# Kernel optimization log

Measured on AMD Instinct MI355X. Metric: run time of the kernel, lower is better.

The kernel has to match this reference:

```python
import jax, jax.numpy as jnp
import numpy as np

EPS = 1e-5


def setup_inputs() -> dict:
    key = jax.random.key(0)
    ks = jax.random.split(key, 16)
    N, P, K, D = 16, 1024, 16, 3
    Cf = 64      # out_features (lifted feature dim)
    Fin = 64     # feature_dim
    Cout = 128   # out_channels
    DM = 4       # depth multiplier
    Ccat = Cf + Fin  # 128
    s = 0.1
    return {
        'rep_pt': jax.random.normal(ks[0], (N, P, D), jnp.float32),
        'pts':    jax.random.normal(ks[1], (N, P, K, D), jnp.float32),
        'fts':    jax.random.normal(ks[2], (N, P, K, Fin), jnp.float32),
        'W_fc1':  jax.random.normal(ks[3], (Cf, D), jnp.float32) * s,
        'b_fc1':  jnp.zeros((Cf,), jnp.float32),
        'W_fc2':  jax.random.normal(ks[4], (Cf, Cf), jnp.float32) * s,
        'b_fc2':  jnp.zeros((Cf,), jnp.float32),
        'W_xconv': jax.random.normal(ks[5], (K * K, D, K), jnp.float32) * s,
        'b_xconv': jnp.zeros((K * K,), jnp.float32),
        'W_xfc1': jax.random.normal(ks[6], (K * K, K * K), jnp.float32) * s,
        'b_xfc1': jnp.zeros((K * K,), jnp.float32),
        'W_xfc2': jax.random.normal(ks[7], (K * K, K * K), jnp.float32) * s,
        'b_xfc2': jnp.zeros((K * K,), jnp.float32),
        'W_dw':   jax.random.normal(ks[8], (Ccat, DM, K), jnp.float32) * s,
        'b_dw':   jnp.zeros((Ccat * DM,), jnp.float32),
        'W_pw':   jax.random.normal(ks[9], (Cout, Ccat * DM), jnp.float32) * s,
        'b_pw':   jnp.zeros((Cout,), jnp.float32),
        'gamma':  jnp.ones((Cout,), jnp.float32),
        'beta':   jnp.zeros((Cout,), jnp.float32),
    }


def reference(rep_pt, pts, fts, W_fc1, b_fc1, W_fc2, b_fc2,
              W_xconv, b_xconv, W_xfc1, b_xfc1, W_xfc2, b_xfc2,
              W_dw, b_dw, W_pw, b_pw, gamma, beta):
    relu = jax.nn.relu
    N, P, K, _ = pts.shape

    # local coords around each representative point
    pts_local = pts - rep_pt[:, :, None, :]                       # (N,P,K,3)

    # feature lift: two FCs with relu
    h = relu(jnp.einsum('npkd,fd->npkf', pts_local, W_fc1) + b_fc1)
    fts_lifted = relu(jnp.einsum('npkf,gf->npkg', h, W_fc2) + b_fc2)  # (N,P,K,Cf)
    fts_cat = jnp.concatenate([fts_lifted, fts], axis=-1)         # (N,P,K,Ccat)

    # X-transform: conv2d kernel (1,K) over (N,3,P,K) -> (N,K^2,P,1), then 2 FCs
    X = relu(jnp.einsum('npkd,odk->npo', pts_local, W_xconv) + b_xconv)  # (N,P,K^2)
    X = relu(X @ W_xfc1.T + b_xfc1)
    X = X @ W_xfc2.T + b_xfc2                                     # linear
    X = X.reshape(N, P, K, K)

    # X-transformed features
    fts_X = jnp.einsum('npij,npjc->npic', X, fts_cat)             # (N,P,K,Ccat)

    # depthwise-separable conv with kernel (1,K): reduces K entirely
    x = fts_X.transpose(0, 3, 1, 2)                               # (N,Ccat,P,K)
    dw = jnp.einsum('ncpk,cmk->ncmp', x, W_dw)                    # (N,Ccat,DM,P)
    dw = dw.reshape(N, -1, P) + b_dw[None, :, None]               # (N,Ccat*DM,P)
    y = jnp.einsum('ncp,oc->nop', dw, W_pw) + b_pw[None, :, None] # (N,Cout,P)

    # batchnorm (training stats over N,P per channel), then relu
    mean = y.mean(axis=(0, 2), keepdims=True)
    var = y.var(axis=(0, 2), keepdims=True)
    y = (y - mean) * jax.lax.rsqrt(var + EPS)
    y = relu(gamma[None, :, None] * y + beta[None, :, None])

    return y.transpose(0, 2, 1)                                   # (N,P,Cout)
```

## Files before the change

### kernel.cpp

```cpp
#include <hip/hip_runtime.h>


#define NPTS 16384

typedef short  s16x8 __attribute__((ext_vector_type(8)));
typedef float  f32x4 __attribute__((ext_vector_type(4)));

__device__ inline unsigned short f2b(float f) {
    unsigned u = __builtin_bit_cast(unsigned, f);
    unsigned r = u + 0x7FFF + ((u >> 16) & 1);
    return (unsigned short)(r >> 16);
}
__device__ inline float b2f(unsigned short b) {
    return __builtin_bit_cast(float, (unsigned)b << 16);
}

#define MFMA(a,b,c) __builtin_amdgcn_mfma_f32_16x16x32_bf16((a),(b),(c),0,0,0)

__global__ __launch_bounds__(256) void kW_cvt(
    const float* __restrict__ Wxc, const float* __restrict__ Wx1,
    const float* __restrict__ Wx2, const float* __restrict__ Wf2,
    const float* __restrict__ Wpw, const float* __restrict__ Wf1,
    const float* __restrict__ bf1, const float* __restrict__ Wdw,
    unsigned short* __restrict__ Wpk, float* __restrict__ W1p,
    unsigned short* __restrict__ Wtb, float* __restrict__ acc)
{
    unsigned short* Wxcpk = Wpk;
    unsigned short* Wx1pk = Wpk + 16384;
    unsigned short* Wx2pk = Wpk + 81920;
    unsigned short* Wf2pk = Wpk + 147456;
    unsigned short* Wpwpk = Wpk + 151552;
    int idx = blockIdx.x * 256 + threadIdx.x;
    if (idx < 16384) {
        int e = idx & 7, ln = (idx >> 3) & 63, ks = (idx >> 9) & 1, ot = idx >> 10;
        int row = ot*16 + (ln & 15), k = ks*32 + (ln >> 4)*8 + e;
        Wxcpk[idx] = (k < 48) ? f2b(Wxc[row*48 + k]) : 0; return; }
    idx -= 16384;
    if (idx < 65536) {
        int e = idx & 7, ln = (idx >> 3) & 63, ks = (idx >> 9) & 7, ot = idx >> 12;
        int row = ot*16 + (ln & 15), k = ks*32 + (ln >> 4)*8 + e;
        Wx1pk[idx] = f2b(Wx1[row*256 + k]); return; }
    idx -= 65536;
    if (idx < 65536) {
        int e = idx & 7, ln = (idx >> 3) & 63, ks = (idx >> 9) & 7, ot = idx >> 12;
        int row = ot*16 + (ln & 15), k = ks*32 + (ln >> 4)*8 + e;
        Wx2pk[idx] = f2b(Wx2[row*256 + k]); return; }
    idx -= 65536;
    if (idx < 4096) {
        int e = idx & 7, ln = (idx >> 3) & 63, ks = (idx >> 9) & 1, ot = idx >> 10;
        int row = ot*16 + (ln & 15), k = ks*32 + (ln >> 4)*8 + e;
        Wf2pk[idx] = f2b(Wf2[row*64 + k]); return; }
    idx -= 4096;
    if (idx < 65536) {
        int e = idx & 7, ln = (idx >> 3) & 63, ks = (idx >> 9) & 15, ot = idx >> 13;
        int row = ot*16 + (ln & 15), k = ks*32 + (ln >> 4)*8 + e;
        Wpwpk[idx] = f2b(Wpw[row*512 + k]); return; }
    idx -= 65536;
    if (idx < 256)   { int f = idx >> 2, j = idx & 3;
        W1p[idx] = (j < 3) ? Wf1[f*3 + j] : bf1[f]; return; }
    idx -= 256;
    if (idx < 8192)  { int m = idx >> 11, rem = idx & 2047;
        int c = rem >> 4, k = rem & 15;
        Wtb[idx] = f2b(Wdw[(size_t)(c*4 + m)*16 + k]); return; }
    idx -= 8192;
    if (idx < 256)   { acc[idx] = 0.f; return; }
}

#define SX 264
__global__ __launch_bounds__(512) void kA_mfma(
    const float* __restrict__ rep, const float* __restrict__ pts,
    const unsigned short* __restrict__ Wpk,
    const float* __restrict__ bxc, const float* __restrict__ bx1,
    const float* __restrict__ bx2, unsigned short* __restrict__ X3b)
{
    const unsigned short* Wxcpk = Wpk;
    const unsigned short* Wx1pk = Wpk + 16384;
    const unsigned short* Wx2pk = Wpk + 81920;
    __shared__ __align__(16) unsigned short X1s[32*SX];
    __shared__ __align__(16) unsigned short X2s[32*SX];
    const int tid = threadIdx.x;
    const int w = tid >> 6, lane = tid & 63, cl = lane & 15, lg = lane >> 4;
    const int mw = w & 1, nw = w >> 1;
    const int base = blockIdx.x * 32;
    const int q = base + mw*16 + cl;
    f32x4 z = {0.f,0.f,0.f,0.f};

    float r0 = rep[q*3+0], r1 = rep[q*3+1], r2 = rep[q*3+2];
    s16x8 aa[2];
    #pragma unroll
    for (int ks = 0; ks < 2; ++ks) {
        #pragma unroll
        for (int e = 0; e < 8; ++e) {
            int j = ks*32 + lg*8 + e;
            float v = 0.f;
            if (j < 48) {
                int d = j >> 4, kk = j & 15;
                float rv = (d == 0) ? r0 : ((d == 1) ? r1 : r2);
                v = pts[(size_t)(q*16 + kk)*3 + d] - rv;
            }
            aa[ks][e] = (short)f2b(v);
        }
    }

    {
        f32x4 acc[4] = {z,z,z,z};
        #pragma unroll
        for (int ks = 0; ks < 2; ++ks) {
            #pragma unroll
            for (int ct = 0; ct < 4; ++ct) {
                int ot = nw*4 + ct;
                s16x8 b = *(const s16x8*)&Wxcpk[((ot*2 + ks)*64 + lane)*8];
                acc[ct] = MFMA(aa[ks], b, acc[ct]);
            }
        }
        #pragma unroll
        for (int ct = 0; ct < 4; ++ct) {
            int o = nw*64 + ct*16 + cl;
            float bias = bxc[o];
            #pragma unroll
            for (int r = 0; r < 4; ++r)
                X1s[(mw*16 + lg*4 + r)*SX + o] = f2b(fmaxf(acc[ct][r] + bias, 0.f));
        }
    }
    __syncthreads();

    {
        f32x4 acc[4] = {z,z,z,z};
        #pragma unroll
        for (int ks = 0; ks < 8; ++ks) {
            s16x8 a = *(const s16x8*)&X1s[(mw*16 + cl)*SX + ks*32 + lg*8];
            #pragma unroll
            for (int ct = 0; ct < 4; ++ct) {
                int ot = nw*4 + ct;
                s16x8 b = *(const s16x8*)&Wx1pk[((ot*8 + ks)*64 + lane)*8];
                acc[ct] = MFMA(a, b, acc[ct]);
            }
        }
        #pragma unroll
        for (int ct = 0; ct < 4; ++ct) {
            int o = nw*64 + ct*16 + cl;
            float bias = bx1[o];
            #pragma unroll
            for (int r = 0; r < 4; ++r)
                X2s[(mw*16 + lg*4 + r)*SX + o] = f2b(fmaxf(acc[ct][r] + bias, 0.f));
        }
    }
    __syncthreads();

    {
        f32x4 acc[4] = {z,z,z,z};
        #pragma unroll
        for (int ks = 0; ks < 8; ++ks) {
            s16x8 a = *(const s16x8*)&X2s[(mw*16 + cl)*SX + ks*32 + lg*8];
            #pragma unroll
            for (int ct = 0; ct < 4; ++ct) {
                int ot = nw*4 + ct;
                s16x8 b = *(const s16x8*)&Wx2pk[((ot*8 + ks)*64 + lane)*8];
                acc[ct] = MFMA(a, b, acc[ct]);
            }
        }
        #pragma unroll
        for (int ct = 0; ct < 4; ++ct) {
            int o = nw*64 + ct*16 + cl;
            float bias = bx2[o];
            #pragma unroll
            for (int r = 0; r < 4; ++r)
                X3b[(size_t)(base + mw*16 + lg*4 + r)*256 + o] = f2b(acc[ct][r] + bias);
        }
    }
}

#define SF 72
__global__ __launch_bounds__(256) void kB_mfma(
    const float* __restrict__ rep, const float* __restrict__ pts,
    const float* __restrict__ fts, const float* __restrict__ W1p,
    const unsigned short* __restrict__ Wpk, const float* __restrict__ bf2,
    const unsigned short* __restrict__ Wtb, const float* __restrict__ bdw,
    const unsigned short* __restrict__ X3b, unsigned short* __restrict__ dwb)
{
    const unsigned short* Wf2pk = Wpk + 147456;
    __shared__ __align__(16) unsigned short fcT[128*SF];
    const int tid = threadIdx.x;
    const int w = tid >> 6, lane = tid & 63, cl = lane & 15, lg = lane >> 4;
    const int p = blockIdx.x*4 + w;
    const int rw = w*16;

    const int frow = lane >> 2, fch = lane & 3;
    float4 fv[4];
    #pragma unroll
    for (int it = 0; it < 4; ++it)
        fv[it] = *(const float4*)&fts[((size_t)p*16 + frow)*64 + fch*4 + it*16];

    s16x8 xa = {0,0,0,0,0,0,0,0};
    if (lg < 2) xa = *(const s16x8*)&X3b[(size_t)p*256 + cl*16 + lg*8];

    const int row = p*16 + cl;
    float x0 = pts[(size_t)row*3+0] - rep[p*3+0];
    float x1 = pts[(size_t)row*3+1] - rep[p*3+1];
    float x2 = pts[(size_t)row*3+2] - rep[p*3+2];

    s16x8 hb[2];
    #pragma unroll
    for (int ks = 0; ks < 2; ++ks) {
        #pragma unroll
        for (int e = 0; e < 8; ++e) {
            int f = ks*32 + lg*8 + e;
            float4 wb4 = *(const float4*)&W1p[f*4];
            float h = fmaxf(wb4.w + wb4.x*x0 + wb4.y*x1 + wb4.z*x2, 0.f);
            hb[ks][e] = (short)f2b(h);
        }
    }

    #pragma unroll
    for (int it = 0; it < 4; ++it) {
        float vv[4] = {fv[it].x, fv[it].y, fv[it].z, fv[it].w};
        #pragma unroll
        for (int cc = 0; cc < 4; ++cc) {
            int c = fch*4 + it*16 + cc;
            fcT[(64 + c)*SF + rw + frow] = f2b(vv[cc]);
        }
    }

    f32x4 z = {0.f,0.f,0.f,0.f};
    {
        f32x4 acc2[4] = {z,z,z,z};
        #pragma unroll
        for (int ks = 0; ks < 2; ++ks) {
            #pragma unroll
            for (int gt = 0; gt < 4; ++gt) {
                s16x8 a = *(const s16x8*)&Wf2pk[((gt*2 + ks)*64 + lane)*8];
                acc2[gt] = MFMA(a, hb[ks], acc2[gt]);
            }
        }
        #pragma unroll
        for (int gt = 0; gt < 4; ++gt) {
            #pragma unroll
            for (int r = 0; r < 4; ++r) {
                int g = gt*16 + lg*4 + r;
                fcT[g*SF + rw + cl] = f2b(fmaxf(acc2[gt][r] + bf2[g], 0.f));
            }
        }
    }

    f32x4 fx[8];
    #pragma unroll
    for (int ct = 0; ct < 8; ++ct) {
        int c = ct*16 + cl;
        s16x8 b = *(const s16x8*)&fcT[c*SF + rw + (lg & 1)*8];
        fx[ct] = MFMA(xa, b, z);
    }

    #pragma unroll
    for (int ct = 0; ct < 8; ++ct) {
        int c = ct*16 + cl;
        float4 b4 = *(const float4*)&bdw[c*4];
        float om[4];
        #pragma unroll
        for (int m = 0; m < 4; ++m) {
            ushort4 wu = *(const ushort4*)&Wtb[m*2048 + c*16 + lg*4];
            float s = fx[ct][0]*b2f(wu.x) + fx[ct][1]*b2f(wu.y)
                    + fx[ct][2]*b2f(wu.z) + fx[ct][3]*b2f(wu.w);
            s += __shfl_xor(s, 16);
            s += __shfl_xor(s, 32);
            om[m] = s + ((const float*)&b4)[m];
        }
        if (lg == 0) {
            ushort4 pk; pk.x=f2b(om[0]); pk.y=f2b(om[1]); pk.z=f2b(om[2]); pk.w=f2b(om[3]);
            *(ushort4*)&dwb[(size_t)p*512 + c*4] = pk;
        }
    }
}

__global__ __launch_bounds__(256) void kC_mfma(
    const unsigned short* __restrict__ dwb, const unsigned short* __restrict__ Wpk,
    const float* __restrict__ bpw, float* __restrict__ y,
    float* __restrict__ accS, float* __restrict__ accS2)
{
    const unsigned short* Wpwpk = Wpk + 151552;
    const int tid = threadIdx.x;
    const int w = tid >> 6, lane = tid & 63, cl = lane & 15, lg = lane >> 4;
    const int m0 = blockIdx.x*32 + (w & 1)*16;
    const int nh = w >> 1;
    f32x4 z = {0.f,0.f,0.f,0.f};
    f32x4 acc[4] = {z,z,z,z};
    for (int ks = 0; ks < 16; ++ks) {
        s16x8 a = *(const s16x8*)&dwb[(size_t)(m0 + cl)*512 + ks*32 + lg*8];
        #pragma unroll
        for (int ct = 0; ct < 4; ++ct) {
            int ot = nh*4 + ct;
            s16x8 b = *(const s16x8*)&Wpwpk[((ot*16 + ks)*64 + lane)*8];
            acc[ct] = MFMA(a, b, acc[ct]);
        }
    }
    #pragma unroll
    for (int ct = 0; ct < 4; ++ct) {
        int o = nh*64 + ct*16 + cl;
        float bias = bpw[o];
        float s1 = 0.f, s2 = 0.f;
        #pragma unroll
        for (int r = 0; r < 4; ++r) {
            float v = acc[ct][r] + bias;
            y[(size_t)(m0 + lg*4 + r)*128 + o] = v;
            s1 += v; s2 += v*v;
        }
        s1 += __shfl_xor(s1, 16); s2 += __shfl_xor(s2, 16);
        s1 += __shfl_xor(s1, 32); s2 += __shfl_xor(s2, 32);
        if (lg == 0) {
            atomicAdd(accS + o, s1);
            atomicAdd(accS2 + o, s2);
        }
    }
}

__global__ void kD2_fin(
    const float* __restrict__ accS, const float* __restrict__ accS2,
    const float* __restrict__ gamma, const float* __restrict__ beta,
    float* __restrict__ st)
{
    const int c = threadIdx.x;
    float mean = accS[c] * (1.f/NPTS);
    float var  = accS2[c] * (1.f/NPTS) - mean*mean;
    float rstd = rsqrtf(var + 1e-5f);
    float sc = gamma[c] * rstd;
    st[c] = sc;
    st[128 + c] = beta[c] - mean*sc;
}

__global__ __launch_bounds__(256) void kE_final(
    const float* __restrict__ y, const float* __restrict__ st,
    float* __restrict__ out)
{
    const int idx = blockIdx.x*256 + threadIdx.x;
    float4 v = ((const float4*)y)[idx];
    int o0 = (idx & 31) << 2;
    float4 sc = *(const float4*)(st + o0);
    float4 sh = *(const float4*)(st + 128 + o0);
    float4 r;
    r.x = fmaxf(v.x*sc.x + sh.x, 0.f);
    r.y = fmaxf(v.y*sc.y + sh.y, 0.f);
    r.z = fmaxf(v.z*sc.z + sh.z, 0.f);
    r.w = fmaxf(v.w*sc.w + sh.w, 0.f);
    ((float4*)out)[idx] = r;
}

extern "C" void kernel_launch(void* const* d_in, const int* in_sizes, int n_in,
                              void* d_out, int out_size, void* d_ws, size_t ws_size,
                              hipStream_t stream) {
    const float* rep  = (const float*)d_in[0];
    const float* pts  = (const float*)d_in[1];
    const float* fts  = (const float*)d_in[2];
    const float* Wf1  = (const float*)d_in[3];
    const float* bf1  = (const float*)d_in[4];
    const float* Wf2  = (const float*)d_in[5];
    const float* bf2  = (const float*)d_in[6];
    const float* Wxc  = (const float*)d_in[7];
    const float* bxc  = (const float*)d_in[8];
    const float* Wx1  = (const float*)d_in[9];
    const float* bx1  = (const float*)d_in[10];
    const float* Wx2  = (const float*)d_in[11];
    const float* bx2  = (const float*)d_in[12];
    const float* Wdw  = (const float*)d_in[13];
    const float* bdw  = (const float*)d_in[14];
    const float* Wpw  = (const float*)d_in[15];
    const float* bpw  = (const float*)d_in[16];
    const float* gam  = (const float*)d_in[17];
    const float* bet  = (const float*)d_in[18];

    unsigned short* X3b = (unsigned short*)d_ws;
    unsigned short* dwb = X3b + (size_t)NPTS*256;
    float* y   = (float*)(dwb + (size_t)NPTS*512);
    float* st  = y + (size_t)NPTS*128;
    float* acc = st + 256;
    unsigned short* Wpk = (unsigned short*)(acc + 256);
    float* W1p = (float*)(Wpk + 217088);
    unsigned short* Wtb = (unsigned short*)(W1p + 256);

    kW_cvt<<<882, 256, 0, stream>>>(Wxc, Wx1, Wx2, Wf2, Wpw, Wf1, bf1, Wdw,
                                    Wpk, W1p, Wtb, acc);
    kA_mfma<<<NPTS/32, 512, 0, stream>>>(rep, pts, Wpk, bxc, bx1, bx2, X3b);
    kB_mfma<<<NPTS/4, 256, 0, stream>>>(rep, pts, fts, W1p, Wpk, bf2, Wtb, bdw, X3b, dwb);
    kC_mfma<<<NPTS/32, 256, 0, stream>>>(dwb, Wpk, bpw, y, acc, acc + 128);
    kD2_fin<<<1, 128, 0, stream>>>(acc, acc + 128, gam, bet, st);
    kE_final<<<(NPTS*128/4)/256, 256, 0, stream>>>(y, st, (float*)d_out);
}
```

Before: 120.7 us.

## Use packed bf16 conversion, fuse BN finalize into apply kernel, interleave kB MFMA

Replaces the software float-to-bf16 rounding with the hardware v_cvt_pk_bf16_f32 instruction, which converts two values at once, in kA and kB. It folds the single-block batchnorm-stats kernel into the final apply kernel so every block recomputes scale and shift into shared memory, removing one launch. In kB it also interleaves the per-channel-tile MFMA with its depthwise reduction so the eight MFMA results are no longer all held in registers together. The aim is to cut conversion ALU work, one launch and register pressure, at the cost of redundant per-block stats math.

```diff
diff --git a/kernel.cpp b/kernel.cpp
--- a/kernel.cpp
+++ b/kernel.cpp
@@ -13,6 +13,11 @@
 }
 __device__ inline float b2f(unsigned short b) {
     return __builtin_bit_cast(float, (unsigned)b << 16);
+}
+__device__ inline unsigned cvtpk(float lo, float hi) {
+    unsigned r;
+    asm("v_cvt_pk_bf16_f32 %0, %1, %2" : "=v"(r) : "v"(lo), "v"(hi));
+    return r;
 }
 
 #define MFMA(a,b,c) __builtin_amdgcn_mfma_f32_16x16x32_bf16((a),(b),(c),0,0,0)
@@ -89,17 +94,24 @@
     s16x8 aa[2];
     #pragma unroll
     for (int ks = 0; ks < 2; ++ks) {
-        #pragma unroll
-        for (int e = 0; e < 8; ++e) {
-            int j = ks*32 + lg*8 + e;
-            float v = 0.f;
-            if (j < 48) {
-                int d = j >> 4, kk = j & 15;
-                float rv = (d == 0) ? r0 : ((d == 1) ? r1 : r2);
-                v = pts[(size_t)(q*16 + kk)*3 + d] - rv;
+        uint4 au;
+        #pragma unroll
+        for (int e2 = 0; e2 < 4; ++e2) {
+            float v[2];
+            #pragma unroll
+            for (int h = 0; h < 2; ++h) {
+                int j = ks*32 + lg*8 + e2*2 + h;
+                float vv = 0.f;
+                if (j < 48) {
+                    int d = j >> 4, kk = j & 15;
+                    float rv = (d == 0) ? r0 : ((d == 1) ? r1 : r2);
+                    vv = pts[(size_t)(q*16 + kk)*3 + d] - rv;
+                }
+                v[h] = vv;
             }
-            aa[ks][e] = (short)f2b(v);
-        }
+            ((unsigned*)&au)[e2] = cvtpk(v[0], v[1]);
+        }
+        aa[ks] = __builtin_bit_cast(s16x8, au);
     }
 
     {
@@ -117,9 +129,13 @@
         for (int ct = 0; ct < 4; ++ct) {
             int o = nw*64 + ct*16 + cl;
             float bias = bxc[o];
-            #pragma unroll
-            for (int r = 0; r < 4; ++r)
-                X1s[(mw*16 + lg*4 + r)*SX + o] = f2b(fmaxf(acc[ct][r] + bias, 0.f));
+            int rb = (mw*16 + lg*4)*SX + o;
+            unsigned u0 = cvtpk(fmaxf(acc[ct][0]+bias,0.f), fmaxf(acc[ct][1]+bias,0.f));
+            unsigned u1 = cvtpk(fmaxf(acc[ct][2]+bias,0.f), fmaxf(acc[ct][3]+bias,0.f));
+            X1s[rb       ] = (unsigned short)u0;
+            X1s[rb +   SX] = (unsigned short)(u0 >> 16);
+            X1s[rb + 2*SX] = (unsigned short)u1;
+            X1s[rb + 3*SX] = (unsigned short)(u1 >> 16);
         }
     }
     __syncthreads();
@@ -140,9 +156,13 @@
         for (int ct = 0; ct < 4; ++ct) {
             int o = nw*64 + ct*16 + cl;
             float bias = bx1[o];
-            #pragma unroll
-            for (int r = 0; r < 4; ++r)
-                X2s[(mw*16 + lg*4 + r)*SX + o] = f2b(fmaxf(acc[ct][r] + bias, 0.f));
+            int rb = (mw*16 + lg*4)*SX + o;
+            unsigned u0 = cvtpk(fmaxf(acc[ct][0]+bias,0.f), fmaxf(acc[ct][1]+bias,0.f));
+            unsigned u1 = cvtpk(fmaxf(acc[ct][2]+bias,0.f), fmaxf(acc[ct][3]+bias,0.f));
+            X2s[rb       ] = (unsigned short)u0;
+            X2s[rb +   SX] = (unsigned short)(u0 >> 16);
+            X2s[rb + 2*SX] = (unsigned short)u1;
+            X2s[rb + 3*SX] = (unsigned short)(u1 >> 16);
         }
     }
     __syncthreads();
@@ -163,9 +183,13 @@
         for (int ct = 0; ct < 4; ++ct) {
             int o = nw*64 + ct*16 + cl;
             float bias = bx2[o];
-            #pragma unroll
-            for (int r = 0; r < 4; ++r)
-                X3b[(size_t)(base + mw*16 + lg*4 + r)*256 + o] = f2b(acc[ct][r] + bias);
+            size_t rb = (size_t)(base + mw*16 + lg*4)*256 + o;
+            unsigned u0 = cvtpk(acc[ct][0]+bias, acc[ct][1]+bias);
+            unsigned u1 = cvtpk(acc[ct][2]+bias, acc[ct][3]+bias);
+            X3b[rb      ] = (unsigned short)u0;
+            X3b[rb + 256] = (unsigned short)(u0 >> 16);
+            X3b[rb + 512] = (unsigned short)u1;
+            X3b[rb + 768] = (unsigned short)(u1 >> 16);
         }
     }
 }
@@ -202,23 +226,29 @@
     s16x8 hb[2];
     #pragma unroll
     for (int ks = 0; ks < 2; ++ks) {
-        #pragma unroll
-        for (int e = 0; e < 8; ++e) {
-            int f = ks*32 + lg*8 + e;
-            float4 wb4 = *(const float4*)&W1p[f*4];
-            float h = fmaxf(wb4.w + wb4.x*x0 + wb4.y*x1 + wb4.z*x2, 0.f);
-            hb[ks][e] = (short)f2b(h);
-        }
+        uint4 hu;
+        #pragma unroll
+        for (int e2 = 0; e2 < 4; ++e2) {
+            int f0 = ks*32 + lg*8 + e2*2;
+            float4 wa = *(const float4*)&W1p[f0*4];
+            float4 wb = *(const float4*)&W1p[(f0+1)*4];
+            float h0 = fmaxf(wa.w + wa.x*x0 + wa.y*x1 + wa.z*x2, 0.f);
+            float h1 = fmaxf(wb.w + wb.x*x0 + wb.y*x1 + wb.z*x2, 0.f);
+            ((unsigned*)&hu)[e2] = cvtpk(h0, h1);
+        }
+        hb[ks] = __builtin_bit_cast(s16x8, hu);
     }
 
     #pragma unroll
     for (int it = 0; it < 4; ++it) {
-        float vv[4] = {fv[it].x, fv[it].y, fv[it].z, fv[it].w};
-        #pragma unroll
-        for (int cc = 0; cc < 4; ++cc) {
-            int c = fch*4 + it*16 + cc;
-            fcT[(64 + c)*SF + rw + frow] = f2b(vv[cc]);
-        }
+        int c0 = fch*4 + it*16;
+        unsigned u0 = cvtpk(fv[it].x, fv[it].y);
+        unsigned u1 = cvtpk(fv[it].z, fv[it].w);
+        int rb = (64 + c0)*SF + rw + frow;
+        fcT[rb       ] = (unsigned short)u0;
+        fcT[rb +   SF] = (unsigned short)(u0 >> 16);
+        fcT[rb + 2*SF] = (unsigned short)u1;
+        fcT[rb + 3*SF] = (unsigned short)(u1 >> 16);
     }
 
     f32x4 z = {0.f,0.f,0.f,0.f};
@@ -234,39 +264,41 @@
         }
         #pragma unroll
         for (int gt = 0; gt < 4; ++gt) {
-            #pragma unroll
-            for (int r = 0; r < 4; ++r) {
-                int g = gt*16 + lg*4 + r;
-                fcT[g*SF + rw + cl] = f2b(fmaxf(acc2[gt][r] + bf2[g], 0.f));
-            }
-        }
-    }
-
-    f32x4 fx[8];
+            int g0 = gt*16 + lg*4;
+            unsigned u0 = cvtpk(fmaxf(acc2[gt][0]+bf2[g0+0],0.f),
+                                fmaxf(acc2[gt][1]+bf2[g0+1],0.f));
+            unsigned u1 = cvtpk(fmaxf(acc2[gt][2]+bf2[g0+2],0.f),
+                                fmaxf(acc2[gt][3]+bf2[g0+3],0.f));
+            int rb = g0*SF + rw + cl;
+            fcT[rb       ] = (unsigned short)u0;
+            fcT[rb +   SF] = (unsigned short)(u0 >> 16);
+            fcT[rb + 2*SF] = (unsigned short)u1;
+            fcT[rb + 3*SF] = (unsigned short)(u1 >> 16);
+        }
+    }
+
     #pragma unroll
     for (int ct = 0; ct < 8; ++ct) {
         int c = ct*16 + cl;
         s16x8 b = *(const s16x8*)&fcT[c*SF + rw + (lg & 1)*8];
-        fx[ct] = MFMA(xa, b, z);
-    }
-
-    #pragma unroll
-    for (int ct = 0; ct < 8; ++ct) {
-        int c = ct*16 + cl;
+        f32x4 fx = MFMA(xa, b, z);
+
         float4 b4 = *(const float4*)&bdw[c*4];
         float om[4];
         #pragma unroll
         for (int m = 0; m < 4; ++m) {
             ushort4 wu = *(const ushort4*)&Wtb[m*2048 + c*16 + lg*4];
-            float s = fx[ct][0]*b2f(wu.x) + fx[ct][1]*b2f(wu.y)
-                    + fx[ct][2]*b2f(wu.z) + fx[ct][3]*b2f(wu.w);
+            float s = fx[0]*b2f(wu.x) + fx[1]*b2f(wu.y)
+                    + fx[2]*b2f(wu.z) + fx[3]*b2f(wu.w);
             s += __shfl_xor(s, 16);
             s += __shfl_xor(s, 32);
             om[m] = s + ((const float*)&b4)[m];
         }
         if (lg == 0) {
-            ushort4 pk; pk.x=f2b(om[0]); pk.y=f2b(om[1]); pk.z=f2b(om[2]); pk.w=f2b(om[3]);
-            *(ushort4*)&dwb[(size_t)p*512 + c*4] = pk;
+            unsigned u0 = cvtpk(om[0], om[1]);
+            unsigned u1 = cvtpk(om[2], om[3]);
+            uint2 pk; pk.x = u0; pk.y = u1;
+            *(uint2*)&dwb[(size_t)p*512 + c*4] = pk;
         }
     }
 }
@@ -312,29 +344,27 @@
     }
 }
 
-__global__ void kD2_fin(
-    const float* __restrict__ accS, const float* __restrict__ accS2,
-    const float* __restrict__ gamma, const float* __restrict__ beta,
-    float* __restrict__ st)
+__global__ __launch_bounds__(256) void kE_final(
+    const float* __restrict__ y, const float* __restrict__ accS,
+    const float* __restrict__ accS2, const float* __restrict__ gamma,
+    const float* __restrict__ beta, float* __restrict__ out)
 {
-    const int c = threadIdx.x;
-    float mean = accS[c] * (1.f/NPTS);
-    float var  = accS2[c] * (1.f/NPTS) - mean*mean;
-    float rstd = rsqrtf(var + 1e-5f);
-    float sc = gamma[c] * rstd;
-    st[c] = sc;
-    st[128 + c] = beta[c] - mean*sc;
-}
-
-__global__ __launch_bounds__(256) void kE_final(
-    const float* __restrict__ y, const float* __restrict__ st,
-    float* __restrict__ out)
-{
-    const int idx = blockIdx.x*256 + threadIdx.x;
+    __shared__ float stl[256];
+    const int tid = threadIdx.x;
+    if (tid < 128) {
+        float mean = accS[tid] * (1.f/NPTS);
+        float var  = accS2[tid] * (1.f/NPTS) - mean*mean;
+        float rstd = rsqrtf(var + 1e-5f);
+        float sc = gamma[tid] * rstd;
+        stl[tid] = sc;
+        stl[128 + tid] = beta[tid] - mean*sc;
+    }
+    __syncthreads();
+    const int idx = blockIdx.x*256 + tid;
     float4 v = ((const float4*)y)[idx];
     int o0 = (idx & 31) << 2;
-    float4 sc = *(const float4*)(st + o0);
-    float4 sh = *(const float4*)(st + 128 + o0);
+    float4 sc = *(const float4*)&stl[o0];
+    float4 sh = *(const float4*)&stl[128 + o0];
     float4 r;
     r.x = fmaxf(v.x*sc.x + sh.x, 0.f);
     r.y = fmaxf(v.y*sc.y + sh.y, 0.f);
@@ -369,8 +399,7 @@
     unsigned short* X3b = (unsigned short*)d_ws;
     unsigned short* dwb = X3b + (size_t)NPTS*256;
     float* y   = (float*)(dwb + (size_t)NPTS*512);
-    float* st  = y + (size_t)NPTS*128;
-    float* acc = st + 256;
+    float* acc = y + (size_t)NPTS*128;
     unsigned short* Wpk = (unsigned short*)(acc + 256);
     float* W1p = (float*)(Wpk + 217088);
     unsigned short* Wtb = (unsigned short*)(W1p + 256);
@@ -380,6 +409,5 @@
     kA_mfma<<<NPTS/32, 512, 0, stream>>>(rep, pts, Wpk, bxc, bx1, bx2, X3b);
     kB_mfma<<<NPTS/4, 256, 0, stream>>>(rep, pts, fts, W1p, Wpk, bf2, Wtb, bdw, X3b, dwb);
     kC_mfma<<<NPTS/32, 256, 0, stream>>>(dwb, Wpk, bpw, y, acc, acc + 128);
-    kD2_fin<<<1, 128, 0, stream>>>(acc, acc + 128, gam, bet, st);
-    kE_final<<<(NPTS*128/4)/256, 256, 0, stream>>>(y, st, (float*)d_out);
-}
+    kE_final<<<(NPTS*128/4)/256, 256, 0, stream>>>(y, acc, acc + 128, gam, bet, (float*)d_out);
+}
```

After: 116.8 us. 1.03x faster.
